# Performance work log

Hardware: AMD Instinct MI355X
Metric: run time of the kernel (lower is better)

Reference implementation:

```python
import jax, jax.numpy as jnp
import numpy as np

N = 50000   # num_nodes
E = 800000  # edges for relation 0
DIN = 512
DOUT = 128


def setup_inputs() -> dict:
    key = jax.random.key(0)
    k1, k2, k3 = jax.random.split(key, 3)
    x = jax.random.normal(k1, (N, DIN), dtype=jnp.float32)
    edge_index = jax.random.randint(k2, (2, E), 0, N, dtype=jnp.int64)
    # GCNConv weight (glorot-ish) and zero bias, as after reset_parameters()
    W = jax.random.normal(k3, (DIN, DOUT), dtype=jnp.float32) * (1.0 / np.sqrt(DIN))
    b = jnp.zeros((DOUT,), dtype=jnp.float32)
    return {"x": x, "edge_index": edge_index, "W": W, "b": b,
            "dropout_probability": 0.5}


def _dropout(h, key, p):
    keep = jax.random.bernoulli(key, 1.0 - p, h.shape)
    return jnp.where(keep, h / (1.0 - p), jnp.zeros((), h.dtype))


def _gcn_conv(h, edge_index, W, b):
    # PyG GCNConv: add self-loops, symmetric normalization, XW then scatter-add.
    src, dst = edge_index[0], edge_index[1]
    loops = jnp.arange(N, dtype=src.dtype)
    col = jnp.concatenate([src, loops])  # gather side (source)
    row = jnp.concatenate([dst, loops])  # scatter side (target)
    ones = jnp.ones(row.shape[0], dtype=h.dtype)
    deg = jax.ops.segment_sum(ones, row, num_segments=N)        # in-degree + 1
    dinv = jnp.where(deg > 0, jax.lax.rsqrt(deg), jnp.zeros((), h.dtype))
    norm = dinv[row] * dinv[col]                                # [E+N]
    hw = h @ W                                                  # [N, DOUT] dense GEMM
    msg = hw[col] * norm[:, None]                               # gather + scale
    out = jax.ops.segment_sum(msg, row, num_segments=N)         # scatter-add
    return out + b


def reference(x, edge_index, W, b, dropout_probability):
    # Forward loop in the source breaks after the first relation, so exactly one
    # conv is applied. training=True dropout with fixed keys for determinism.
    p = dropout_probability
    k1, k2, k3 = jax.random.split(jax.random.key(1), 3)

    pos_seq = _dropout(x, k1, p)
    pos_h = jax.nn.relu(_gcn_conv(pos_seq, edge_index, W, b))
    summary = jax.nn.sigmoid(jnp.mean(pos_h, axis=0, keepdims=True))

    neg_seq = _dropout(x, k2, p)
    perm = jax.random.permutation(k3, N)   # torch.randperm corruption
    neg_h = jax.nn.relu(_gcn_conv(neg_seq[perm], edge_index, W, b))

    return (pos_h, neg_h, summary, pos_seq, neg_seq)
```

## Files before the change

kernel.cpp:

```cpp
#include <hip/hip_runtime.h>
#include <stdint.h>

static constexpr int    N_NODES = 50000;
static constexpr int    N_EDGES = 800000;
static constexpr int    DIN     = 512;
static constexpr int    DOUT    = 128;
static constexpr size_t SEQ_ELEMS = (size_t)N_NODES * DIN;
static constexpr size_t H_ELEMS   = (size_t)N_NODES * DOUT;

static constexpr int RS_NB = 49;
static constexpr int EDGE_BLOCKS = 782;

typedef __attribute__((ext_vector_type(8))) short bf16x8;
typedef __attribute__((ext_vector_type(4))) float f32x4;
typedef __attribute__((ext_vector_type(4))) unsigned short u16x4;

static constexpr size_t W_HDR    = 0;
static constexpr size_t W_DEGCNT = 16;
static constexpr size_t W_CURSOR = 50016;
static constexpr size_t W_SUMBUF = 100016;
static constexpr size_t W_CNT    = 100144;
static constexpr size_t W_ZEND   = 100152;
static constexpr size_t W_HIST   = 100152;
static constexpr size_t W_OFFS   = 150328;
static constexpr size_t W_ROWPTR = 175416;
static constexpr size_t W_COLSRC = 225420;
static constexpr size_t W_DINV   = 1025420;
static constexpr size_t W_KEYS   = 1075420;
static constexpr size_t W_VALS   = 1275420;
static constexpr size_t W_RANK   = 1475420;
static constexpr size_t W_PERM   = 1575420;
static constexpr size_t W_BT     = 1625420;
static constexpr size_t W_HWPOS  = 1658188;
static constexpr size_t W_HWNEG  = 4858188;

__device__ __forceinline__ uint16_t f2bf(float f) {
  uint32_t u = __float_as_uint(f);
  return (uint16_t)((u + 0x7FFFu + ((u >> 16) & 1u)) >> 16);
}
__device__ __forceinline__ float b2f(uint16_t h) {
  return __uint_as_float(((uint32_t)h) << 16);
}
__device__ __forceinline__ uint32_t rotl32(uint32_t x, int r) {
  return (x << r) | (x >> (32 - r));
}

__device__ __forceinline__ void threefry2x32(uint32_t k0, uint32_t k1,
                                             uint32_t x0, uint32_t x1,
                                             uint32_t& o0, uint32_t& o1) {
  uint32_t ks0 = k0, ks1 = k1, ks2 = k0 ^ k1 ^ 0x1BD11BDAu;
  x0 += ks0; x1 += ks1;
#define TF_ROUND(r) { x0 += x1; x1 = rotl32(x1, (r)); x1 ^= x0; }
  TF_ROUND(13) TF_ROUND(15) TF_ROUND(26) TF_ROUND(6)
  x0 += ks1; x1 += ks2 + 1u;
  TF_ROUND(17) TF_ROUND(29) TF_ROUND(16) TF_ROUND(24)
  x0 += ks2; x1 += ks0 + 2u;
  TF_ROUND(13) TF_ROUND(15) TF_ROUND(26) TF_ROUND(6)
  x0 += ks0; x1 += ks1 + 3u;
  TF_ROUND(17) TF_ROUND(29) TF_ROUND(16) TF_ROUND(24)
  x0 += ks1; x1 += ks2 + 4u;
  TF_ROUND(13) TF_ROUND(15) TF_ROUND(26) TF_ROUND(6)
  x0 += ks2; x1 += ks0 + 5u;
#undef TF_ROUND
  o0 = x0; o1 = x1;
}

__device__ __forceinline__ uint32_t randbits32(uint32_t k0, uint32_t k1, uint32_t ctr) {
  uint32_t a, b;
  threefry2x32(k0, k1, 0u, ctr, a, b);
  return a ^ b;
}

__global__ void __launch_bounds__(256) wt_init_kernel(const float* __restrict__ W,
                                                      uint32_t* __restrict__ wsu) {
  {
    int gid = blockIdx.x * 256 + threadIdx.x;
    for (size_t i = W_DEGCNT + gid; i < W_ZEND; i += 4096) wsu[i] = 0u;
  }
  if (blockIdx.x == 0 && threadIdx.x == 0) {
    uint32_t k3a, k3b, ra, rb, s1a, s1b, s2a, s2b;
    threefry2x32(0u, 1u, 0u, 2u, k3a, k3b);
    threefry2x32(k3a, k3b, 0u, 0u, ra, rb);
    threefry2x32(k3a, k3b, 0u, 1u, s1a, s1b);
    threefry2x32(ra, rb, 0u, 1u, s2a, s2b);
    wsu[4] = s1a; wsu[5] = s1b; wsu[6] = s2a; wsu[7] = s2b;
  }
  uint16_t* BT = (uint16_t*)(wsu + W_BT);
  __shared__ float tile[32][129];
  int k0 = blockIdx.x * 32;
  int t = threadIdx.x;
  for (int i = t; i < 32 * 128; i += 256) {
    int k = i >> 7, n = i & 127;
    tile[k][n] = W[(size_t)(k0 + k) * DOUT + n];
  }
  __syncthreads();
  for (int i = t; i < 32 * 128; i += 256) {
    int n = i >> 5, k = i & 31;
    BT[(size_t)n * DIN + k0 + k] = f2bf(tile[k][n]);
  }
}

__global__ void __launch_bounds__(1024) fusedA_kernel(const int* __restrict__ ei,
                                                      uint32_t* __restrict__ wsu) {
  int b = blockIdx.x;
  if (b < EDGE_BLOCKS) {
    int e = b * 1024 + threadIdx.x;
    if (e < N_EDGES) atomicAdd(&wsu[W_DEGCNT + ei[N_EDGES + e]], 1u);
  } else {
    __shared__ uint32_t h[256];
    int sb = b - EDGE_BLOCKS, s = sb / RS_NB, bb = sb % RS_NB;
    int t = threadIdx.x;
    if (t < 256) h[t] = 0u;
    __syncthreads();
    uint32_t k0 = wsu[4 + 2 * s], k1 = wsu[5 + 2 * s];
    int p = bb * 1024 + t;
    if (p < N_NODES) {
      uint32_t kv = randbits32(k0, k1, (uint32_t)p);
      wsu[W_KEYS + (size_t)s * 100000 + p] = kv;
      wsu[W_VALS + (size_t)s * 100000 + p] = (uint32_t)p;
      atomicAdd(&h[kv & 255u], 1u);
    }
    __syncthreads();
    if (t < 256) wsu[W_HIST + (size_t)s * 25088 + t * RS_NB + bb] = h[t];
  }
}

__device__ __forceinline__ void scan12544(const uint32_t* __restrict__ hist,
                                          uint32_t* __restrict__ offs,
                                          uint32_t* __restrict__ zeroT,
                                          uint32_t* __restrict__ sc) {
  const int t = threadIdx.x;
  int c0 = t * 13, c1 = c0 + 13;
  if (c0 > 12544) c0 = 12544;
  if (c1 > 12544) c1 = 12544;
  uint32_t loc[13];
  uint32_t sum = 0;
  for (int c = c0; c < c1; ++c) {
    uint32_t v = hist[c];
    loc[c - c0] = v;
    sum += v;
  }
  sc[t] = sum;
  __syncthreads();
  for (int off = 1; off < 1024; off <<= 1) {
    uint32_t xx = (t >= off) ? sc[t - off] : 0u;
    __syncthreads();
    sc[t] += xx;
    __syncthreads();
  }
  uint32_t run = sc[t] - sum;
  for (int c = c0; c < c1; ++c) {
    offs[c] = run;
    run += loc[c - c0];
  }
  if (zeroT != nullptr)
    for (int i = t; i < 12544; i += 1024) zeroT[i] = 0u;
}

__global__ void __launch_bounds__(1024) fusedB_kernel(uint32_t* __restrict__ wsu) {
  __shared__ uint32_t sc[1024];
  int b = blockIdx.x, t = threadIdx.x;
  if (b == 0) {
    int c0 = t * 49, c1 = c0 + 49;
    if (c0 > N_NODES) c0 = N_NODES;
    if (c1 > N_NODES) c1 = N_NODES;
    float* dinv = (float*)(wsu + W_DINV);
    uint32_t sum = 0;
    for (int c = c0; c < c1; ++c) {
      uint32_t v = wsu[W_DEGCNT + c];
      dinv[c] = __frsqrt_rn((float)(v + 1u));
      sum += v;
    }
    sc[t] = sum;
    __syncthreads();
    for (int off = 1; off < 1024; off <<= 1) {
      uint32_t xx = (t >= off) ? sc[t - off] : 0u;
      __syncthreads();
      sc[t] += xx;
      __syncthreads();
    }
    uint32_t run = sc[t] - sum;
    for (int c = c0; c < c1; ++c) {
      uint32_t h = wsu[W_DEGCNT + c];
      wsu[W_ROWPTR + c] = run;
      run += h;
    }
    if (t == 0) wsu[W_ROWPTR + N_NODES] = (uint32_t)N_EDGES;
  } else {
    int s = b - 1;
    scan12544(wsu + W_HIST + (size_t)s * 25088, wsu + W_OFFS + (size_t)s * 12544,
              wsu + W_HIST + (size_t)s * 25088 + 12544, sc);
  }
}

__global__ void __launch_bounds__(1024) fill_kernel(const int* __restrict__ ei,
                                                    uint32_t* __restrict__ wsu) {
  int e = blockIdx.x * 1024 + threadIdx.x;
  if (e < N_EDGES) {
    int src = ei[e], dst = ei[N_EDGES + e];
    uint32_t pos = wsu[W_ROWPTR + dst] + atomicAdd(&wsu[W_CURSOR + dst], 1u);
    wsu[W_COLSRC + pos] = (uint32_t)src;
  }
}

template <int PASS>
__global__ void __launch_bounds__(1024) scat_kernel(uint32_t* __restrict__ wsu) {
  __shared__ uint32_t gh[4096];
  const int b = blockIdx.x;
  const int s = b / RS_NB, bb = b % RS_NB;
  const int t = threadIdx.x;
  constexpr int shift = PASS * 8;
  const uint32_t* ki = wsu + W_KEYS + (size_t)s * 100000 + (PASS & 1) * 50000;
  const uint32_t* vi = wsu + W_VALS + (size_t)s * 100000 + (PASS & 1) * 50000;
  uint32_t* ko = wsu + W_KEYS + (size_t)s * 100000 + ((PASS + 1) & 1) * 50000;
  uint32_t* vo = wsu + W_VALS + (size_t)s * 100000 + ((PASS + 1) & 1) * 50000;
  const uint32_t* offs = wsu + W_OFFS + (size_t)s * 12544;
  uint32_t* histN = wsu + W_HIST + (size_t)s * 25088 + ((PASS + 1) & 1) * 12544;
  uint32_t* rank = wsu + W_RANK + (size_t)s * 50000;

  for (int i = t; i < 4096; i += 1024) gh[i] = 0u;
  __syncthreads();
  const int w = t >> 6, l = t & 63;
  const uint64_t pre = (1ull << l) - 1ull;
  int p = bb * 1024 + t;
  bool valid = p < N_NODES;
  uint32_t kv = valid ? ki[p] : 0u;
  uint32_t d = (kv >> shift) & 255u;
  uint64_t m = __ballot(valid);
#pragma unroll
  for (int bit = 0; bit < 8; ++bit) {
    uint64_t bbm = __ballot((d >> bit) & 1u);
    m &= ((d >> bit) & 1u) ? bbm : ~bbm;
  }
  int peer = __popcll(m & pre);
  if (valid && peer == 0) gh[w * 256 + d] = (uint32_t)__popcll(m);
  __syncthreads();
  if (t < 256) {
    uint32_t run = 0;
#pragma unroll
    for (int g = 0; g < 16; ++g) {
      uint32_t tmp = gh[g * 256 + t];
      gh[g * 256 + t] = run;
      run += tmp;
    }
  }
  __syncthreads();
  if (valid) {
    uint32_t pos = offs[d * RS_NB + bb] + gh[w * 256 + d] + (uint32_t)peer;
    uint32_t pv = vi[p];
    if constexpr (PASS == 3) {
      if (pv < (uint32_t)N_NODES && pos < (uint32_t)N_NODES)
        rank[pv] = pos;
    } else {
      if (pos < (uint32_t)N_NODES) {
        ko[pos] = kv;
        vo[pos] = pv;
        atomicAdd(&histN[((kv >> (shift + 8)) & 255u) * RS_NB + (pos >> 10)], 1u);
      }
    }
  }
}

template <int PASS>
__global__ void __launch_bounds__(1024) scan_kernel(uint32_t* __restrict__ wsu) {
  __shared__ uint32_t sc[1024];
  int s = blockIdx.x;
  const uint32_t* h = wsu + W_HIST + (size_t)s * 25088 + (PASS & 1) * 12544;
  uint32_t* of = wsu + W_OFFS + (size_t)s * 12544;
  uint32_t* z = (PASS < 3) ? (wsu + W_HIST + (size_t)s * 25088 + ((PASS + 1) & 1) * 12544)
                           : nullptr;
  scan12544(h, of, z, sc);
}

__global__ void __launch_bounds__(1024) invperm_kernel(uint32_t* __restrict__ wsu) {
  int j = blockIdx.x * 1024 + threadIdx.x;
  if (j < N_NODES) {
    uint32_t r1 = wsu[W_RANK + j];
    uint32_t r2 = (r1 < (uint32_t)N_NODES) ? wsu[W_RANK + 50000 + r1] : 0u;
    wsu[W_PERM + j] = (r2 < (uint32_t)N_NODES) ? r2 : 0u;
  }
}

__global__ void __launch_bounds__(256) dg_kernel(const float* __restrict__ x,
                                                 const uint16_t* __restrict__ BT,
                                                 const float* __restrict__ pprob,
                                                 const float* __restrict__ dinv,
                                                 const uint32_t* __restrict__ invp,
                                                 float* __restrict__ seq_pos,
                                                 float* __restrict__ seq_neg,
                                                 uint16_t* __restrict__ hw_pos,
                                                 uint16_t* __restrict__ hw_neg, int M) {
  __shared__ __align__(16) uint16_t ldsA[64 * 64];
  __shared__ __align__(16) uint16_t ldsB[128 * 64];
  const int which = blockIdx.y;
  float*    seq = which ? seq_neg : seq_pos;
  uint16_t* hwb = which ? hw_neg : hw_pos;

  uint32_t kk0, kk1;
  threefry2x32(0u, 1u, 0u, (uint32_t)which, kk0, kk1);
  const float p = pprob[0];
  const float keep_p = 1.0f - p;
  const float scale  = 1.0f / keep_p;
  uint32_t Tint = (uint32_t)ceilf(keep_p * 8388608.0f);
  uint32_t Tu = (Tint >= (1u << 23)) ? 0xFFFFFFFFu : (Tint << 9);

  const int tid  = threadIdx.x;
  const int lane = tid & 63;
  const int w    = tid >> 6;
  const int wr   = w >> 1, wc = w & 1;
  const int m0   = blockIdx.x * 64;
  const int l15  = lane & 15, l4 = lane >> 4;
  const int lr   = lane >> 3, lk = (lane & 7) * 8;

  f32x4 acc[2][4] = {};

  for (int k0 = 0; k0 < DIN; k0 += 64) {
#pragma unroll
    for (int s = 0; s < 4; ++s) {
      int nbase = w * 32 + s * 8;
      const uint16_t* gp = BT + (size_t)(nbase + lr) * DIN + k0 + lk;
      __builtin_amdgcn_global_load_lds(
          (const __attribute__((address_space(1))) void*)gp,
          (__attribute__((address_space(3))) void*)(ldsB + nbase * 64), 16, 0, 0);
    }
#pragma unroll
    for (int i = 0; i < 4; ++i) {
      int idx = tid + i * 256;
      int row = idx >> 4, q = idx & 15;
      int grow = m0 + row;
      bool valid = grow < M;
      int crow = valid ? grow : (M - 1);
      float4 v = *reinterpret_cast<const float4*>(x + (size_t)crow * DIN + k0 + q * 4);
      float r[4] = {v.x, v.y, v.z, v.w};
      uint32_t cbase = (uint32_t)crow * DIN + k0 + q * 4;
#pragma unroll
      for (int j = 0; j < 4; ++j) {
        uint32_t bits = randbits32(kk0, kk1, cbase + j);
        r[j] = (bits < Tu) ? r[j] * scale : 0.0f;
      }
      if (valid)
        *reinterpret_cast<float4*>(seq + (size_t)grow * DIN + k0 + q * 4) =
            make_float4(r[0], r[1], r[2], r[3]);
      uint32_t u0 = __float_as_uint(r[0]), u1 = __float_as_uint(r[1]);
      uint32_t lo = (u0 >> 16) | (u1 & 0xFFFF0000u);
      u0 = __float_as_uint(r[2]); u1 = __float_as_uint(r[3]);
      uint32_t hi = (u0 >> 16) | (u1 & 0xFFFF0000u);
      *reinterpret_cast<uint2*>(&ldsA[row * 64 + q * 4]) = make_uint2(lo, hi);
    }
    asm volatile("s_waitcnt vmcnt(0)" ::: "memory");
    __syncthreads();
#pragma unroll
    for (int kk = 0; kk < 2; ++kk) {
      bf16x8 afr[2], bfr[4];
#pragma unroll
      for (int f = 0; f < 2; ++f)
        afr[f] = *reinterpret_cast<const bf16x8*>(ldsA + (wr * 32 + f * 16 + l15) * 64 + kk * 32 + l4 * 8);
#pragma unroll
      for (int f = 0; f < 4; ++f)
        bfr[f] = *reinterpret_cast<const bf16x8*>(ldsB + (wc * 64 + f * 16 + l15) * 64 + kk * 32 + l4 * 8);
#pragma unroll
      for (int fm = 0; fm < 2; ++fm)
#pragma unroll
        for (int fn = 0; fn < 4; ++fn)
          acc[fm][fn] = __builtin_amdgcn_mfma_f32_16x16x32_bf16(afr[fm], bfr[fn], acc[fm][fn], 0, 0, 0);
    }
    __syncthreads();
  }
#pragma unroll
  for (int fm = 0; fm < 2; ++fm) {
#pragma unroll
    for (int r = 0; r < 4; ++r) {
      int row = m0 + wr * 32 + fm * 16 + l4 * 4 + r;
      if (row < M) {
        uint32_t slot = which ? invp[row] : (uint32_t)row;
        float sc = dinv[slot];
        uint16_t* cp = hwb + (size_t)slot * DOUT + wc * 64 + l15;
#pragma unroll
        for (int fn = 0; fn < 4; ++fn)
          cp[fn * 16] = f2bf(acc[fm][fn][r] * sc);
      }
    }
  }
}

__global__ void __launch_bounds__(256) gcn_gather_kernel(const uint16_t* __restrict__ hwP,
                                                         const uint16_t* __restrict__ hwN,
                                                         const float* __restrict__ dinv,
                                                         const uint32_t* __restrict__ rowptr,
                                                         const uint32_t* __restrict__ colsrc,
                                                         const float* __restrict__ bias,
                                                         float* __restrict__ out_pos,
                                                         float* __restrict__ out_neg) {
  int node = blockIdx.x * 8 + (threadIdx.x >> 5);
  if (node >= N_NODES) return;
  int c4 = (threadIdx.x & 31) * 4;
  uint32_t e0 = rowptr[node], e1 = rowptr[node + 1];
  float px = 0.f, py = 0.f, pz = 0.f, pw = 0.f;
  float nx = 0.f, ny = 0.f, nz = 0.f, nw = 0.f;
  for (uint32_t e = e0; e < e1; ++e) {
    uint32_t s = colsrc[e];
    u16x4 vp = *reinterpret_cast<const u16x4*>(hwP + (size_t)s * DOUT + c4);
    u16x4 vn = *reinterpret_cast<const u16x4*>(hwN + (size_t)s * DOUT + c4);
    px += b2f(vp.x); py += b2f(vp.y); pz += b2f(vp.z); pw += b2f(vp.w);
    nx += b2f(vn.x); ny += b2f(vn.y); nz += b2f(vn.z); nw += b2f(vn.w);
  }
  u16x4 sp = *reinterpret_cast<const u16x4*>(hwP + (size_t)node * DOUT + c4);
  u16x4 sn = *reinterpret_cast<const u16x4*>(hwN + (size_t)node * DOUT + c4);
  float4 bv = *reinterpret_cast<const float4*>(bias + c4);
  float dn = dinv[node];
  float4 op, on;
  op.x = fmaxf(dn * (px + b2f(sp.x)) + bv.x, 0.0f);
  op.y = fmaxf(dn * (py + b2f(sp.y)) + bv.y, 0.0f);
  op.z = fmaxf(dn * (pz + b2f(sp.z)) + bv.z, 0.0f);
  op.w = fmaxf(dn * (pw + b2f(sp.w)) + bv.w, 0.0f);
  on.x = fmaxf(dn * (nx + b2f(sn.x)) + bv.x, 0.0f);
  on.y = fmaxf(dn * (ny + b2f(sn.y)) + bv.y, 0.0f);
  on.z = fmaxf(dn * (nz + b2f(sn.z)) + bv.z, 0.0f);
  on.w = fmaxf(dn * (nw + b2f(sn.w)) + bv.w, 0.0f);
  *reinterpret_cast<float4*>(out_pos + (size_t)node * DOUT + c4) = op;
  *reinterpret_cast<float4*>(out_neg + (size_t)node * DOUT + c4) = on;
}

__global__ void __launch_bounds__(128) colsum_sig_kernel(const float* __restrict__ ph,
                                                         float* __restrict__ sumbuf,
                                                         uint32_t* __restrict__ counter,
                                                         float* __restrict__ outs) {
  int c = threadIdx.x;
  int r0 = blockIdx.x * 256;
  int r1 = r0 + 256; if (r1 > N_NODES) r1 = N_NODES;
  float s = 0.0f;
  for (int r = r0; r < r1; ++r) s += ph[(size_t)r * DOUT + c];
  atomicAdd(&sumbuf[c], s);
  __threadfence();
  __syncthreads();
  __shared__ uint32_t lastflag;
  if (c == 0) lastflag = atomicAdd(counter, 1u);
  __syncthreads();
  if (lastflag == gridDim.x - 1) {
    __threadfence();
    float m = atomicAdd(&sumbuf[c], 0.0f) * (1.0f / (float)N_NODES);
    outs[c] = 1.0f / (1.0f + expf(-m));
  }
}

extern "C" void kernel_launch(void* const* d_in, const int* in_sizes, int n_in,
                              void* d_out, int out_size, void* d_ws, size_t ws_size,
                              hipStream_t stream) {
  const float* x     = (const float*)d_in[0];
  const int*   ei    = (const int*)d_in[1];
  const float* W     = (const float*)d_in[2];
  const float* bias  = (const float*)d_in[3];
  const float* pprob = (const float*)d_in[4];

  float* out = (float*)d_out;
  float* out_pos_h   = out;
  float* out_neg_h   = out + H_ELEMS;
  float* out_summary = out + 2 * H_ELEMS;
  float* out_pos_seq = out + 2 * H_ELEMS + DOUT;
  float* out_neg_seq = out_pos_seq + SEQ_ELEMS;

  uint32_t* wsu    = (uint32_t*)d_ws;
  float*    sumbuf = (float*)(wsu + W_SUMBUF);
  uint32_t* rowptr = wsu + W_ROWPTR;
  uint32_t* colsrc = wsu + W_COLSRC;
  float*    dinv   = (float*)(wsu + W_DINV);
  uint32_t* invp   = wsu + W_PERM;
  uint16_t* BT     = (uint16_t*)(wsu + W_BT);
  uint16_t* hw_pos = (uint16_t*)(wsu + W_HWPOS);
  uint16_t* hw_neg = (uint16_t*)(wsu + W_HWNEG);

  wt_init_kernel<<<DIN / 32, 256, 0, stream>>>(W, wsu);

  fusedA_kernel<<<EDGE_BLOCKS + 2 * RS_NB, 1024, 0, stream>>>(ei, wsu);

  fusedB_kernel<<<3, 1024, 0, stream>>>(wsu);

  fill_kernel<<<EDGE_BLOCKS, 1024, 0, stream>>>(ei, wsu);

  scat_kernel<0><<<2 * RS_NB, 1024, 0, stream>>>(wsu);
  scan_kernel<1><<<2, 1024, 0, stream>>>(wsu);
  scat_kernel<1><<<2 * RS_NB, 1024, 0, stream>>>(wsu);
  scan_kernel<2><<<2, 1024, 0, stream>>>(wsu);
  scat_kernel<2><<<2 * RS_NB, 1024, 0, stream>>>(wsu);
  scan_kernel<3><<<2, 1024, 0, stream>>>(wsu);
  scat_kernel<3><<<2 * RS_NB, 1024, 0, stream>>>(wsu);

  invperm_kernel<<<RS_NB, 1024, 0, stream>>>(wsu);

  dim3 dgrid((N_NODES + 63) / 64, 2);
  dg_kernel<<<dgrid, 256, 0, stream>>>(x, BT, pprob, dinv, invp,
                                       out_pos_seq, out_neg_seq, hw_pos, hw_neg, N_NODES);

  gcn_gather_kernel<<<(N_NODES + 7) / 8, 256, 0, stream>>>(hw_pos, hw_neg, dinv, rowptr,
                                                           colsrc, bias, out_pos_h, out_neg_h);

  colsum_sig_kernel<<<(N_NODES + 255) / 256, 128, 0, stream>>>(out_pos_h, sumbuf,
                                                               wsu + W_CNT + 3, out_summary);

  (void)in_sizes; (void)n_in; (void)out_size; (void)ws_size;
}
```

Measured before the change: 581.7 us.

## Fuse column-sum sigmoid into gather, unroll edge loop, relax GEMM waits

The separate colsum_sig kernel is folded into the gather kernel. Each block reduces its relu outputs into shared memory and does one global atomic per column, with a last-block sigmoid finalize. The gather edge loop is unrolled by four so more independent global loads are in flight. The dropout GEMM kernel replaces __syncthreads with raw s_barrier plus sched barriers and waits with vmcnt(4) instead of vmcnt(0). That partial wait only holds if the four LDS-direct B loads complete before the later seq stores, which is an ordering assumption. The fusion also adds 6250 blocks of global atomics on 128 addresses.

```diff
diff --git a/kernel.cpp b/kernel.cpp
--- a/kernel.cpp
+++ b/kernel.cpp
@@ -10,6 +10,7 @@
 
 static constexpr int RS_NB = 49;
 static constexpr int EDGE_BLOCKS = 782;
+static_assert(N_NODES % 8 == 0, "gather grid assumes 8 nodes/block exactly");
 
 typedef __attribute__((ext_vector_type(8))) short bf16x8;
 typedef __attribute__((ext_vector_type(4))) float f32x4;
@@ -323,13 +324,13 @@
           (const __attribute__((address_space(1))) void*)gp,
           (__attribute__((address_space(3))) void*)(ldsB + nbase * 64), 16, 0, 0);
     }
+    __builtin_amdgcn_sched_barrier(0);
 #pragma unroll
     for (int i = 0; i < 4; ++i) {
       int idx = tid + i * 256;
       int row = idx >> 4, q = idx & 15;
       int grow = m0 + row;
-      bool valid = grow < M;
-      int crow = valid ? grow : (M - 1);
+      int crow = (grow < M) ? grow : (M - 1);
       float4 v = *reinterpret_cast<const float4*>(x + (size_t)crow * DIN + k0 + q * 4);
       float r[4] = {v.x, v.y, v.z, v.w};
       uint32_t cbase = (uint32_t)crow * DIN + k0 + q * 4;
@@ -338,17 +339,17 @@
         uint32_t bits = randbits32(kk0, kk1, cbase + j);
         r[j] = (bits < Tu) ? r[j] * scale : 0.0f;
       }
-      if (valid)
-        *reinterpret_cast<float4*>(seq + (size_t)grow * DIN + k0 + q * 4) =
-            make_float4(r[0], r[1], r[2], r[3]);
+      *reinterpret_cast<float4*>(seq + (size_t)crow * DIN + k0 + q * 4) =
+          make_float4(r[0], r[1], r[2], r[3]);
       uint32_t u0 = __float_as_uint(r[0]), u1 = __float_as_uint(r[1]);
       uint32_t lo = (u0 >> 16) | (u1 & 0xFFFF0000u);
       u0 = __float_as_uint(r[2]); u1 = __float_as_uint(r[3]);
       uint32_t hi = (u0 >> 16) | (u1 & 0xFFFF0000u);
       *reinterpret_cast<uint2*>(&ldsA[row * 64 + q * 4]) = make_uint2(lo, hi);
     }
-    asm volatile("s_waitcnt vmcnt(0)" ::: "memory");
-    __syncthreads();
+    asm volatile("s_waitcnt vmcnt(4) lgkmcnt(0)" ::: "memory");
+    __builtin_amdgcn_s_barrier();
+    __builtin_amdgcn_sched_barrier(0);
 #pragma unroll
     for (int kk = 0; kk < 2; ++kk) {
       bf16x8 afr[2], bfr[4];
@@ -364,7 +365,7 @@
         for (int fn = 0; fn < 4; ++fn)
           acc[fm][fn] = __builtin_amdgcn_mfma_f32_16x16x32_bf16(afr[fm], bfr[fn], acc[fm][fn], 0, 0, 0);
     }
-    __syncthreads();
+    __builtin_amdgcn_s_barrier();
   }
 #pragma unroll
   for (int fm = 0; fm < 2; ++fm) {
@@ -390,14 +391,41 @@
                                                          const uint32_t* __restrict__ colsrc,
                                                          const float* __restrict__ bias,
                                                          float* __restrict__ out_pos,
-                                                         float* __restrict__ out_neg) {
-  int node = blockIdx.x * 8 + (threadIdx.x >> 5);
-  if (node >= N_NODES) return;
-  int c4 = (threadIdx.x & 31) * 4;
+                                                         float* __restrict__ out_neg,
+                                                         float* __restrict__ sumbuf,
+                                                         uint32_t* __restrict__ counter,
+                                                         float* __restrict__ outs) {
+  __shared__ float csum[128];
+  const int t = threadIdx.x;
+  if (t < 128) csum[t] = 0.0f;
+  __syncthreads();
+
+  int node = blockIdx.x * 8 + (t >> 5);
+  int c4 = (t & 31) * 4;
   uint32_t e0 = rowptr[node], e1 = rowptr[node + 1];
   float px = 0.f, py = 0.f, pz = 0.f, pw = 0.f;
   float nx = 0.f, ny = 0.f, nz = 0.f, nw = 0.f;
-  for (uint32_t e = e0; e < e1; ++e) {
+  uint32_t e = e0;
+  for (; e + 4 <= e1; e += 4) {
+    uint32_t s0 = colsrc[e], s1 = colsrc[e + 1], s2 = colsrc[e + 2], s3 = colsrc[e + 3];
+    u16x4 p0 = *reinterpret_cast<const u16x4*>(hwP + (size_t)s0 * DOUT + c4);
+    u16x4 p1 = *reinterpret_cast<const u16x4*>(hwP + (size_t)s1 * DOUT + c4);
+    u16x4 p2 = *reinterpret_cast<const u16x4*>(hwP + (size_t)s2 * DOUT + c4);
+    u16x4 p3 = *reinterpret_cast<const u16x4*>(hwP + (size_t)s3 * DOUT + c4);
+    u16x4 n0 = *reinterpret_cast<const u16x4*>(hwN + (size_t)s0 * DOUT + c4);
+    u16x4 n1 = *reinterpret_cast<const u16x4*>(hwN + (size_t)s1 * DOUT + c4);
+    u16x4 n2 = *reinterpret_cast<const u16x4*>(hwN + (size_t)s2 * DOUT + c4);
+    u16x4 n3 = *reinterpret_cast<const u16x4*>(hwN + (size_t)s3 * DOUT + c4);
+    px += (b2f(p0.x) + b2f(p1.x)) + (b2f(p2.x) + b2f(p3.x));
+    py += (b2f(p0.y) + b2f(p1.y)) + (b2f(p2.y) + b2f(p3.y));
+    pz += (b2f(p0.z) + b2f(p1.z)) + (b2f(p2.z) + b2f(p3.z));
+    pw += (b2f(p0.w) + b2f(p1.w)) + (b2f(p2.w) + b2f(p3.w));
+    nx += (b2f(n0.x) + b2f(n1.x)) + (b2f(n2.x) + b2f(n3.x));
+    ny += (b2f(n0.y) + b2f(n1.y)) + (b2f(n2.y) + b2f(n3.y));
+    nz += (b2f(n0.z) + b2f(n1.z)) + (b2f(n2.z) + b2f(n3.z));
+    nw += (b2f(n0.w) + b2f(n1.w)) + (b2f(n2.w) + b2f(n3.w));
+  }
+  for (; e < e1; ++e) {
     uint32_t s = colsrc[e];
     u16x4 vp = *reinterpret_cast<const u16x4*>(hwP + (size_t)s * DOUT + c4);
     u16x4 vn = *reinterpret_cast<const u16x4*>(hwN + (size_t)s * DOUT + c4);
@@ -419,27 +447,22 @@
   on.w = fmaxf(dn * (nw + b2f(sn.w)) + bv.w, 0.0f);
   *reinterpret_cast<float4*>(out_pos + (size_t)node * DOUT + c4) = op;
   *reinterpret_cast<float4*>(out_neg + (size_t)node * DOUT + c4) = on;
-}
-
-__global__ void __launch_bounds__(128) colsum_sig_kernel(const float* __restrict__ ph,
-                                                         float* __restrict__ sumbuf,
-                                                         uint32_t* __restrict__ counter,
-                                                         float* __restrict__ outs) {
-  int c = threadIdx.x;
-  int r0 = blockIdx.x * 256;
-  int r1 = r0 + 256; if (r1 > N_NODES) r1 = N_NODES;
-  float s = 0.0f;
-  for (int r = r0; r < r1; ++r) s += ph[(size_t)r * DOUT + c];
-  atomicAdd(&sumbuf[c], s);
+
+  atomicAdd(&csum[c4 + 0], op.x);
+  atomicAdd(&csum[c4 + 1], op.y);
+  atomicAdd(&csum[c4 + 2], op.z);
+  atomicAdd(&csum[c4 + 3], op.w);
+  __syncthreads();
+  if (t < 128) atomicAdd(&sumbuf[t], csum[t]);
   __threadfence();
   __syncthreads();
   __shared__ uint32_t lastflag;
-  if (c == 0) lastflag = atomicAdd(counter, 1u);
-  __syncthreads();
-  if (lastflag == gridDim.x - 1) {
+  if (t == 0) lastflag = atomicAdd(counter, 1u);
+  __syncthreads();
+  if (lastflag == gridDim.x - 1 && t < 128) {
     __threadfence();
-    float m = atomicAdd(&sumbuf[c], 0.0f) * (1.0f / (float)N_NODES);
-    outs[c] = 1.0f / (1.0f + expf(-m));
+    float mv = atomicAdd(&sumbuf[t], 0.0f) * (1.0f / (float)N_NODES);
+    outs[t] = 1.0f / (1.0f + expf(-mv));
   }
 }
 
@@ -491,11 +514,9 @@
   dg_kernel<<<dgrid, 256, 0, stream>>>(x, BT, pprob, dinv, invp,
                                        out_pos_seq, out_neg_seq, hw_pos, hw_neg, N_NODES);
 
-  gcn_gather_kernel<<<(N_NODES + 7) / 8, 256, 0, stream>>>(hw_pos, hw_neg, dinv, rowptr,
-                                                           colsrc, bias, out_pos_h, out_neg_h);
-
-  colsum_sig_kernel<<<(N_NODES + 255) / 256, 128, 0, stream>>>(out_pos_h, sumbuf,
-                                                               wsu + W_CNT + 3, out_summary);
+  gcn_gather_kernel<<<N_NODES / 8, 256, 0, stream>>>(hw_pos, hw_neg, dinv, rowptr,
+                                                     colsrc, bias, out_pos_h, out_neg_h,
+                                                     sumbuf, wsu + W_CNT + 3, out_summary);
 
   (void)in_sizes; (void)n_in; (void)out_size; (void)ws_size;
 }
```

After: 1.267 ms. 2.18x slower.
